# Kernel optimization log

Hardware: AMD Instinct MI355X
Metric: run time of the kernel (lower is better)

## Reference

```python
import jax, jax.numpy as jnp
import numpy as np

N, D, HID, IN_DIM, ED = 8192, 16, 128, 128, 8


def _lin(k, fi, fo):
    return jax.random.normal(k, (fi, fo), jnp.float32) / np.sqrt(fi).astype(np.float32)


def setup_inputs() -> dict:
    key = jax.random.key(0)
    ks = jax.random.split(key, 8)
    rng = np.random.default_rng(0)
    # DAG with topological order 0..N-1: node v in [1,N) gets D predecessors in [0, v)
    v_arr = np.arange(1, N)
    src = np.floor(rng.random((N - 1, D)) * v_arr[:, None]).astype(np.int64)  # [N-1, D]
    dst = np.repeat(v_arr, D)
    edge_index = jnp.asarray(np.stack([src.reshape(-1), dst]))  # [2, E]
    E = (N - 1) * D
    return {
        "x": jax.random.normal(ks[0], (N, IN_DIM), jnp.float32),
        "edge_index": edge_index,
        "edge_attr": jax.random.normal(ks[1], (E, ED), jnp.float32),
        "Wp": _lin(ks[2], IN_DIM, HID), "bp": jnp.zeros(HID, jnp.float32),
        "Wm1": _lin(ks[3], HID + ED, HID), "bm1": jnp.zeros(HID, jnp.float32),
        "Wm2": _lin(ks[4], HID, HID), "bm2": jnp.zeros(HID, jnp.float32),
        "Wu1": _lin(ks[5], 2 * HID, HID), "bu1": jnp.zeros(HID, jnp.float32),
        "Wu2": _lin(ks[6], HID, HID), "bu2": jnp.zeros(HID, jnp.float32),
    }


def _build_struct(edge_index, num_nodes):
    # Group edges by destination, padded to max in-degree (host-side, int constants)
    si, di = np.asarray(edge_index)
    order = np.argsort(di, kind="stable")
    si_s, di_s = si[order], di[order]
    deg = np.bincount(di_s, minlength=num_nodes)
    Dm = max(int(deg.max()), 1)
    offs = np.concatenate([[0], np.cumsum(deg)])
    pos = np.arange(di_s.shape[0]) - offs[di_s]  # slot of each edge within its dst group
    src_pad = np.zeros((num_nodes, Dm), np.int64)
    mask = np.zeros((num_nodes, Dm), np.float32)
    src_pad[di_s, pos] = si_s
    mask[di_s, pos] = 1.0
    return (jnp.asarray(src_pad), jnp.asarray(mask),
            jnp.asarray(order), jnp.asarray(di_s), jnp.asarray(pos), Dm)


def _forward(x, edge_attr, params, struct):
    Wp, bp, Wm1, bm1, Wm2, bm2, Wu1, bu1, Wu2, bu2 = params
    src_pad, mask, order, di_s, pos, Dm = struct
    num_nodes = x.shape[0]
    relu = jax.nn.relu
    # Scatter edge attrs into padded [N, Dm, ED] slots (differentiable w.r.t. edge_attr)
    attr_pad = jnp.zeros((num_nodes, Dm, edge_attr.shape[-1]), edge_attr.dtype)
    attr_pad = attr_pad.at[di_s, pos].set(edge_attr[order])
    h0 = x @ Wp + bp  # node_proj

    def step(h, inp):
        srcs, attr, m, v = inp
        hs = h[srcs]                                    # [Dm, HID] current (possibly updated) states
        z = jnp.concatenate([hs, attr], axis=-1)        # [Dm, HID+ED]
        msgs = relu(relu(z @ Wm1 + bm1) @ Wm2 + bm2)    # msg_mlp
        cnt = m.sum()
        agg = (msgs * m[:, None]).sum(0) / jnp.maximum(cnt, 1.0)  # masked mean
        cat = jnp.concatenate([h[v], agg])              # [2*HID]
        new = relu(relu(cat @ Wu1 + bu1) @ Wu2 + bu2)   # update_mlp
        h = h.at[v].set(jnp.where(cnt > 0, new, h[v]))  # skip nodes with no in-edges
        return h, None

    h, _ = jax.lax.scan(step, h0, (src_pad, attr_pad, mask, jnp.arange(num_nodes)))
    return h


def reference(x, edge_index, edge_attr, Wp, bp, Wm1, bm1, Wm2, bm2, Wu1, bu1, Wu2, bu2):
    struct = _build_struct(edge_index, x.shape[0])
    params = (Wp, bp, Wm1, bm1, Wm2, bm2, Wu1, bu1, Wu2, bu2)
    return _forward(x, edge_attr, params, struct)
```

## Files before the change

kernel.cpp:

```cpp
#include <hip/hip_runtime.h>

#define NN   8192
#define DEG  16
#define HID  128
#define IND  128
#define ED   8
#define NBLK 256

typedef __bf16 bf16_t;
typedef __bf16 bf16x8 __attribute__((ext_vector_type(8)));
typedef float  f32x4  __attribute__((ext_vector_type(4)));
typedef unsigned long long u64;

static __device__ __forceinline__ f32x4 mfma16(bf16x8 a, bf16x8 b, f32x4 c) {
  return __builtin_amdgcn_mfma_f32_16x16x32_bf16(a, b, c, 0, 0, 0);
}
static __device__ __forceinline__ unsigned short bfbits(bf16_t x) {
  return __builtin_bit_cast(unsigned short, x);
}
static __device__ __forceinline__ bf16_t bits2bf(unsigned short x) {
  return __builtin_bit_cast(bf16_t, x);
}
static __device__ __forceinline__ void bar_lds() {
  __builtin_amdgcn_sched_barrier(0);
  asm volatile("s_waitcnt lgkmcnt(0)" ::: "memory");
  __builtin_amdgcn_s_barrier();
  __builtin_amdgcn_sched_barrier(0);
}
static __device__ __forceinline__ void bar_full() {
  __builtin_amdgcn_sched_barrier(0);
  asm volatile("s_waitcnt vmcnt(0) lgkmcnt(0)" ::: "memory");
  __builtin_amdgcn_s_barrier();
  __builtin_amdgcn_sched_barrier(0);
}

__global__ __launch_bounds__(128) void k_h0(const float* __restrict__ x,
                                            const float* __restrict__ Wp,
                                            const float* __restrict__ bp,
                                            float* __restrict__ h,
                                            unsigned* __restrict__ h2u,
                                            int* __restrict__ flags, int fs,
                                            int sent) {
  __shared__ float sx[8][IND];
  const int t  = threadIdx.x;
  const int vb = blockIdx.x * 8;
  #pragma unroll
  for (int rr = 0; rr < 8; ++rr) sx[rr][t] = x[(size_t)(vb + rr) * IND + t];
  __syncthreads();
  float acc[8];
  const float bias = bp[t];
  #pragma unroll
  for (int rr = 0; rr < 8; ++rr) acc[rr] = bias;
  for (int k = 0; k < IND; ++k) {
    const float w = Wp[k * HID + t];
    #pragma unroll
    for (int rr = 0; rr < 8; ++rr) acc[rr] += sx[rr][k] * w;
  }
  #pragma unroll
  for (int rr = 0; rr < 8; ++rr) h[(size_t)(vb + rr) * HID + t] = acc[rr];
  if (sent) {
    #pragma unroll
    for (int rr = 0; rr < 8; ++rr) {
      unsigned val = 0xFFFFFFFFu;
      if (vb + rr == 0) {
        const float f = acc[rr];
        const bf16_t fh = (bf16_t)f;
        const bf16_t fl = (bf16_t)(f - (float)fh);
        val = ((unsigned)bfbits(fh) << 16) | (unsigned)bfbits(fl);
      }
      h2u[(size_t)(vb + rr) * HID + t] = val;
    }
  } else if (t < 8) {
    flags[(vb + t) * fs] = (vb + t == 0) ? 0xF : 0;
  }
}

#define LOAD_WFRAGS(W, KROWS, NKK, ARRH, ARRL)                                \
  _Pragma("unroll")                                                           \
  for (int n = 0; n < 2; ++n) {                                               \
    _Pragma("unroll")                                                         \
    for (int kk = 0; kk < NKK; ++kk) {                                        \
      _Pragma("unroll")                                                       \
      for (int i = 0; i < 8; ++i) {                                           \
        const int k = kk * 32 + g * 8 + i;                                    \
        const float w = (k < KROWS) ? W[k * HID + cc[n]] : 0.f;               \
        const bf16_t wh = (bf16_t)w;                                          \
        ARRH[n][kk][i] = wh;                                                  \
        ARRL[n][kk][i] = (bf16_t)(w - (float)wh);                             \
      }                                                                       \
    }                                                                         \
  }
#define LOAD_WFRAGS_H(W, KROWS, NKK, ARRH)                                    \
  _Pragma("unroll")                                                           \
  for (int n = 0; n < 2; ++n) {                                               \
    _Pragma("unroll")                                                         \
    for (int kk = 0; kk < NKK; ++kk) {                                        \
      _Pragma("unroll")                                                       \
      for (int i = 0; i < 8; ++i) {                                           \
        const int k = kk * 32 + g * 8 + i;                                    \
        const float w = (k < KROWS) ? W[k * HID + cc[n]] : 0.f;               \
        ARRH[n][kk][i] = (bf16_t)w;                                           \
      }                                                                       \
    }                                                                         \
  }

#define LOADQ()                                                               \
  _Pragma("unroll")                                                           \
  for (int kk = 0; kk < 4; ++kk) {                                            \
    _Pragma("unroll")                                                         \
    for (int u = 0; u < 4; ++u)                                               \
      q[kk * 4 + u] = __hip_atomic_load(hp + kk * 16 + u, __ATOMIC_RELAXED,   \
                                        __HIP_MEMORY_SCOPE_AGENT);            \
  }

#define ZERO4(a) { a[0][0]=0.f;a[0][1]=0.f;a[0][2]=0.f;a[0][3]=0.f; a[1]=a[0]; }
#define BIAS4(a, b) { a[0][0]=b[0];a[0][1]=b[0];a[0][2]=b[0];a[0][3]=b[0];    \
                      a[1][0]=b[1];a[1][1]=b[1];a[1][2]=b[1];a[1][3]=b[1]; }

template <bool SENT>
__global__ __launch_bounds__(256, 1) void k_dag(
    const int* __restrict__ ei, const float* __restrict__ attr,
    const float* __restrict__ Wm1, const float* __restrict__ bm1,
    const float* __restrict__ Wm2, const float* __restrict__ bm2,
    const float* __restrict__ Wu1, const float* __restrict__ bu1,
    const float* __restrict__ Wu2, const float* __restrict__ bu2,
    float* __restrict__ h, unsigned* __restrict__ h2u,
    int* __restrict__ flags, int fs) {
  const int tid  = threadIdx.x;
  const int lane = tid & 63;
  const int g    = lane >> 4;
  const int r    = lane & 15;
  const int wid  = tid >> 6;

  __shared__ bf16_t s_m1[16 * HID];
  __shared__ alignas(16) bf16_t s_agg[HID];
  __shared__ alignas(16) bf16_t s_u1[HID];

  int cc[2];
  cc[0] = wid * 32 + 2 * r;
  cc[1] = cc[0] + 1;

  bf16x8 wm1h[2][5], wm1l[2][5];
  bf16x8 wm2h[2][4];
  bf16x8 wu1h[2][8], wu1l[2][4];
  bf16x8 wu2h[2][4], wu2l[2][4];
  LOAD_WFRAGS(Wm1, 136, 5, wm1h, wm1l)
  LOAD_WFRAGS_H(Wm2, 128, 4, wm2h)
  LOAD_WFRAGS_H(Wu1, 256, 8, wu1h)
  LOAD_WFRAGS(Wu1, 128, 4, wu1h , wu1l)
  LOAD_WFRAGS(Wu2, 128, 4, wu2h, wu2l)
  float bs_m1[2], bs_m2[2], bs_u1[2], bs_u2[2];
  #pragma unroll
  for (int n = 0; n < 2; ++n) {
    bs_m1[n] = bm1[cc[n]]; bs_m2[n] = bm2[cc[n]];
    bs_u1[n] = bu1[cc[n]]; bs_u2[n] = bu2[cc[n]];
  }

  const int v0 = 1 + (int)blockIdx.x;
  int s_cur = (v0 < NN) ? ei[(v0 - 1) * DEG + r] : 0;

  for (int v = v0; v < NN; v += NBLK) {
    u64 q[16];
    const u64* hp =
        (const u64*)((SENT ? (const void*)h2u : (const void*)h)) +
        (size_t)s_cur * (HID / 2) + g * 4;
    LOADQ();

    const int vn = (v + NBLK < NN) ? v + NBLK : v;
    const int s_nxt = ei[(vn - 1) * DEG + r];

    bf16x8 hvh[4], hvl[4];
    {
      const float* hvp = h + (size_t)v * HID + g * 8;
      #pragma unroll
      for (int kk = 0; kk < 4; ++kk) {
        const f32x4 p0 = *(const f32x4*)(hvp + kk * 32);
        const f32x4 p1 = *(const f32x4*)(hvp + kk * 32 + 4);
        #pragma unroll
        for (int i = 0; i < 4; ++i) {
          const float f0 = p0[i], f1 = p1[i];
          const bf16_t f0h = (bf16_t)f0, f1h = (bf16_t)f1;
          hvh[kk][i]     = f0h; hvl[kk][i]     = (bf16_t)(f0 - (float)f0h);
          hvh[kk][4 + i] = f1h; hvl[kk][4 + i] = (bf16_t)(f1 - (float)f1h);
        }
      }
    }
    bf16x8 a4h;
    #pragma unroll
    for (int i = 0; i < 8; ++i) a4h[i] = (bf16_t)0.f;
    if (g == 0) {
      const f32x4* ap = (const f32x4*)(attr + ((size_t)(v - 1) * DEG + r) * ED);
      const f32x4 a0 = ap[0], a1 = ap[1];
      #pragma unroll
      for (int i = 0; i < 4; ++i) {
        a4h[i] = (bf16_t)a0[i]; a4h[4 + i] = (bf16_t)a1[i];
      }
    }

    f32x4 uA[2], uB[2], uC[2], uD[2];
    BIAS4(uA, bs_u1) ZERO4(uB) ZERO4(uC) ZERO4(uD)
    #pragma unroll
    for (int kk = 0; kk < 4; ++kk) {
      #pragma unroll
      for (int n = 0; n < 2; ++n) {
        uA[n] = mfma16(hvh[kk], wu1h[n][kk], uA[n]);
        uB[n] = mfma16(hvh[kk], wu1l[n][kk], uB[n]);
        uC[n] = mfma16(hvl[kk], wu1h[n][kk], uC[n]);
      }
    }
    f32x4 mA[2], mB[2], mC[2], mD[2], mE[2], mF[2];
    BIAS4(mA, bs_m1) ZERO4(mB) ZERO4(mC) ZERO4(mD) ZERO4(mE) ZERO4(mF)
    #pragma unroll
    for (int n = 0; n < 2; ++n) {
      mA[n] = mfma16(a4h, wm1h[n][4], mA[n]);
      mB[n] = mfma16(a4h, wm1l[n][4], mB[n]);
    }

    if constexpr (SENT) {
      bool ok = false;
      int guard = 0;
      for (;;) {
        if (!ok) {
          u64 m = 0;
          #pragma unroll
          for (int i = 0; i < 16; ++i) m |= q[i];
          ok = (s_cur == 0) || ((m & 0x8000000080000000ull) == 0);
        }
        if (__all(ok)) break;
        if (++guard > (1 << 13)) break;
        if (!ok) LOADQ();
      }
    } else {
      const int* fp = flags + s_cur * fs;
      int fw = __hip_atomic_load(fp, __ATOMIC_RELAXED, __HIP_MEMORY_SCOPE_AGENT);
      int guard = 0;
      while (fw != 0xF && ++guard < (1 << 15)) {
        __builtin_amdgcn_s_sleep(1);
        fw = __hip_atomic_load(fp, __ATOMIC_RELAXED, __HIP_MEMORY_SCOPE_AGENT);
      }
      asm volatile("" ::: "memory");
      LOADQ();
    }

    bf16x8 ah[4], al[4];
    #pragma unroll
    for (int kk = 0; kk < 4; ++kk) {
      #pragma unroll
      for (int u = 0; u < 4; ++u) {
        #pragma unroll
        for (int b = 0; b < 2; ++b) {
          const unsigned w = (unsigned)(q[kk * 4 + u] >> (32 * b));
          if constexpr (SENT) {
            ah[kk][u * 2 + b] = bits2bf((unsigned short)(w >> 16));
            al[kk][u * 2 + b] = bits2bf((unsigned short)(w & 0xFFFFu));
          } else {
            const float f = __uint_as_float(w);
            const bf16_t fh = (bf16_t)f;
            ah[kk][u * 2 + b] = fh;
            al[kk][u * 2 + b] = (bf16_t)(f - (float)fh);
          }
        }
      }
    }

    f32x4 m1[2];
    #pragma unroll
    for (int kk = 0; kk < 2; ++kk) {
      #pragma unroll
      for (int n = 0; n < 2; ++n) {
        mA[n] = mfma16(ah[kk], wm1h[n][kk], mA[n]);
        mB[n] = mfma16(ah[kk], wm1l[n][kk], mB[n]);
        mC[n] = mfma16(al[kk], wm1h[n][kk], mC[n]);
        mD[n] = mfma16(ah[kk + 2], wm1h[n][kk + 2], mD[n]);
        mE[n] = mfma16(ah[kk + 2], wm1l[n][kk + 2], mE[n]);
        mF[n] = mfma16(al[kk + 2], wm1h[n][kk + 2], mF[n]);
      }
    }
    #pragma unroll
    for (int n = 0; n < 2; ++n)
      m1[n] = ((mA[n] + mB[n]) + (mC[n] + mD[n])) + (mE[n] + mF[n]);
    #pragma unroll
    for (int n = 0; n < 2; ++n) {
      const int c = cc[n], ch16 = c >> 3;
      #pragma unroll
      for (int reg = 0; reg < 4; ++reg) {
        const int j = g * 4 + reg;
        s_m1[j * HID + ((ch16 ^ j) * 8) + (c & 7)] = (bf16_t)fmaxf(m1[n][reg], 0.f);
      }
    }
    if constexpr (SENT) bar_lds(); else __syncthreads();

    f32x4 m2[2];
    {
      f32x4 aA[2], aC[2];
      BIAS4(aA, bs_m2) ZERO4(aC)
      #pragma unroll
      for (int kk = 0; kk < 2; ++kk) {
        const int ph0 = (kk * 4 + g) ^ r;
        const int ph1 = ((kk + 2) * 4 + g) ^ r;
        const bf16x8 a0 = *(const bf16x8*)(s_m1 + r * HID + ph0 * 8);
        const bf16x8 a1 = *(const bf16x8*)(s_m1 + r * HID + ph1 * 8);
        #pragma unroll
        for (int n = 0; n < 2; ++n) {
          aA[n] = mfma16(a0, wm2h[n][kk], aA[n]);
          aC[n] = mfma16(a1, wm2h[n][kk + 2], aC[n]);
        }
      }
      #pragma unroll
      for (int n = 0; n < 2; ++n) m2[n] = aA[n] + aC[n];
    }
    #pragma unroll
    for (int n = 0; n < 2; ++n) {
      float s = fmaxf(m2[n][0],0.f)+fmaxf(m2[n][1],0.f)+fmaxf(m2[n][2],0.f)+fmaxf(m2[n][3],0.f);
      s += __shfl_xor(s, 16, 64);
      s += __shfl_xor(s, 32, 64);
      if (lane < 16) s_agg[cc[n]] = (bf16_t)(s * 0.0625f);
    }
    if constexpr (SENT) bar_lds(); else __syncthreads();

    f32x4 u1v[2];
    #pragma unroll
    for (int kk = 4; kk < 6; ++kk) {
      const bf16x8 Ah0 = *(const bf16x8*)(s_agg + (kk - 4) * 32 + g * 8);
      const bf16x8 Ah1 = *(const bf16x8*)(s_agg + (kk - 2) * 32 + g * 8);
      #pragma unroll
      for (int n = 0; n < 2; ++n) {
        uA[n] = mfma16(Ah0, wu1h[n][kk], uA[n]);
        uD[n] = mfma16(Ah1, wu1h[n][kk + 2], uD[n]);
      }
    }
    #pragma unroll
    for (int n = 0; n < 2; ++n)
      u1v[n] = (uA[n] + uB[n]) + (uC[n] + uD[n]);
    if (lane < 16) {
      s_u1[cc[0]] = (bf16_t)fmaxf(u1v[0][0], 0.f);
      s_u1[cc[1]] = (bf16_t)fmaxf(u1v[1][0], 0.f);
    }
    if constexpr (SENT) bar_lds(); else __syncthreads();

    f32x4 u2v[2];
    {
      f32x4 aA[2], aB[2], aC[2], aD[2];
      BIAS4(aA, bs_u2) ZERO4(aB) ZERO4(aC) ZERO4(aD)
      #pragma unroll
      for (int kk = 0; kk < 2; ++kk) {
        const bf16x8 Ah0 = *(const bf16x8*)(s_u1 + kk * 32 + g * 8);
        const bf16x8 Ah1 = *(const bf16x8*)(s_u1 + (kk + 2) * 32 + g * 8);
        #pragma unroll
        for (int n = 0; n < 2; ++n) {
          aA[n] = mfma16(Ah0, wu2h[n][kk], aA[n]);
          aB[n] = mfma16(Ah0, wu2l[n][kk], aB[n]);
          aC[n] = mfma16(Ah1, wu2h[n][kk + 2], aC[n]);
          aD[n] = mfma16(Ah1, wu2l[n][kk + 2], aD[n]);
        }
      }
      #pragma unroll
      for (int n = 0; n < 2; ++n) u2v[n] = (aA[n] + aB[n]) + (aC[n] + aD[n]);
    }
    if (lane < 16) {
      if constexpr (SENT) {
        u64 pp = 0;
        #pragma unroll
        for (int n = 0; n < 2; ++n) {
          const float rv = fabsf(fmaxf(u2v[n][0], 0.f));
          const bf16_t rh = (bf16_t)rv;
          const bf16_t rl = (bf16_t)(rv - (float)rh);
          const unsigned pw = ((unsigned)bfbits(rh) << 16) | (unsigned)bfbits(rl);
          pp |= (u64)pw << (32 * n);
        }
        __hip_atomic_store((u64*)&h2u[(size_t)v * HID + cc[0]], pp,
                           __ATOMIC_RELAXED, __HIP_MEMORY_SCOPE_AGENT);
      } else {
        #pragma unroll
        for (int n = 0; n < 2; ++n) {
          const float rv = fabsf(fmaxf(u2v[n][0], 0.f));
          __hip_atomic_store(&h[(size_t)v * HID + cc[n]], rv,
                             __ATOMIC_RELAXED, __HIP_MEMORY_SCOPE_AGENT);
        }
      }
    }
    if constexpr (!SENT) {
      if (lane == 0)
        __hip_atomic_fetch_or(&flags[v * fs], 1 << wid, __ATOMIC_RELEASE,
                              __HIP_MEMORY_SCOPE_AGENT);
    }
    s_cur = s_nxt;
    if constexpr (!SENT) __syncthreads();
  }

  if constexpr (SENT) {
    bar_full();
    const int half = tid >> 7;
    const int c    = tid & 127;
    #pragma unroll 4
    for (int v = v0 + half * NBLK; v < NN; v += 2 * NBLK) {
      const unsigned w = __hip_atomic_load(&h2u[(size_t)v * HID + c],
                                           __ATOMIC_RELAXED,
                                           __HIP_MEMORY_SCOPE_AGENT);
      h[(size_t)v * HID + c] =
          (float)bits2bf((unsigned short)(w >> 16)) +
          (float)bits2bf((unsigned short)(w & 0xFFFFu));
    }
  }
}

extern "C" void kernel_launch(void* const* d_in, const int* in_sizes, int n_in,
                              void* d_out, int out_size, void* d_ws, size_t ws_size,
                              hipStream_t stream) {
  const float* x    = (const float*)d_in[0];
  const int*   ei   = (const int*)  d_in[1];
  const float* attr = (const float*)d_in[2];
  const float* Wp   = (const float*)d_in[3];
  const float* bp   = (const float*)d_in[4];
  const float* Wm1  = (const float*)d_in[5];
  const float* bm1  = (const float*)d_in[6];
  const float* Wm2  = (const float*)d_in[7];
  const float* bm2  = (const float*)d_in[8];
  const float* Wu1  = (const float*)d_in[9];
  const float* bu1  = (const float*)d_in[10];
  const float* Wu2  = (const float*)d_in[11];
  const float* bu2  = (const float*)d_in[12];
  float* h = (float*)d_out;

  const size_t h2_bytes = (size_t)NN * HID * sizeof(unsigned);
  const bool sent = ws_size >= h2_bytes;
  unsigned* h2u = (unsigned*)d_ws;
  int* flags    = (int*)d_ws;
  const int fs = sent ? 0 : ((ws_size >= (size_t)NN * 64 + 64) ? 16 : 1);

  k_h0<<<NN / 8, 128, 0, stream>>>(x, Wp, bp, h, h2u, flags, fs, sent ? 1 : 0);
  if (sent)
    k_dag<true><<<NBLK, 256, 0, stream>>>(ei, attr, Wm1, bm1, Wm2, bm2,
                                          Wu1, bu1, Wu2, bu2, h, h2u, flags, fs);
  else
    k_dag<false><<<NBLK, 256, 0, stream>>>(ei, attr, Wm1, bm1, Wm2, bm2,
                                           Wu1, bu1, Wu2, bu2, h, h2u, flags, fs);
}
```

Before: 556.1 us.

## Split hi/lo bf16 planes and drop low-part gather in message matmul

```diff
diff --git a/kernel.cpp b/kernel.cpp
--- a/kernel.cpp
+++ b/kernel.cpp
@@ -11,6 +11,7 @@
 typedef __bf16 bf16x8 __attribute__((ext_vector_type(8)));
 typedef float  f32x4  __attribute__((ext_vector_type(4)));
 typedef unsigned long long u64;
+typedef u64 u64x2 __attribute__((ext_vector_type(2)));
 
 static __device__ __forceinline__ f32x4 mfma16(bf16x8 a, bf16x8 b, f32x4 c) {
   return __builtin_amdgcn_mfma_f32_16x16x32_bf16(a, b, c, 0, 0, 0);
@@ -38,7 +39,8 @@
                                             const float* __restrict__ Wp,
                                             const float* __restrict__ bp,
                                             float* __restrict__ h,
-                                            unsigned* __restrict__ h2u,
+                                            bf16_t* __restrict__ h2hi,
+                                            bf16_t* __restrict__ h2lo,
                                             int* __restrict__ flags, int fs,
                                             int sent) {
   __shared__ float sx[8][IND];
@@ -61,14 +63,15 @@
   if (sent) {
     #pragma unroll
     for (int rr = 0; rr < 8; ++rr) {
-      unsigned val = 0xFFFFFFFFu;
+      unsigned short hw = 0xFFFFu, lw = 0xFFFFu;
       if (vb + rr == 0) {
         const float f = acc[rr];
         const bf16_t fh = (bf16_t)f;
-        const bf16_t fl = (bf16_t)(f - (float)fh);
-        val = ((unsigned)bfbits(fh) << 16) | (unsigned)bfbits(fl);
-      }
-      h2u[(size_t)(vb + rr) * HID + t] = val;
+        hw = bfbits(fh);
+        lw = bfbits((bf16_t)(f - (float)fh));
+      }
+      h2hi[(size_t)(vb + rr) * HID + t] = bits2bf(hw);
+      h2lo[(size_t)(vb + rr) * HID + t] = bits2bf(lw);
     }
   } else if (t < 8) {
     flags[(vb + t) * fs] = (vb + t == 0) ? 0xF : 0;
@@ -103,13 +106,26 @@
       }                                                                       \
     }                                                                         \
   }
-
-#define LOADQ()                                                               \
+#define LOAD_WFRAGS_L(W, KROWS, NKK, ARRL)                                    \
+  _Pragma("unroll")                                                           \
+  for (int n = 0; n < 2; ++n) {                                               \
+    _Pragma("unroll")                                                         \
+    for (int kk = 0; kk < NKK; ++kk) {                                        \
+      _Pragma("unroll")                                                       \
+      for (int i = 0; i < 8; ++i) {                                           \
+        const int k = kk * 32 + g * 8 + i;                                    \
+        const float w = (k < KROWS) ? W[k * HID + cc[n]] : 0.f;               \
+        ARRL[n][kk][i] = (bf16_t)(w - (float)(bf16_t)w);                      \
+      }                                                                       \
+    }                                                                         \
+  }
+
+#define LOADQH()                                                              \
   _Pragma("unroll")                                                           \
   for (int kk = 0; kk < 4; ++kk) {                                            \
     _Pragma("unroll")                                                         \
-    for (int u = 0; u < 4; ++u)                                               \
-      q[kk * 4 + u] = __hip_atomic_load(hp + kk * 16 + u, __ATOMIC_RELAXED,   \
+    for (int u = 0; u < 2; ++u)                                               \
+      q[kk * 2 + u] = __hip_atomic_load(hp + kk * 8 + u, __ATOMIC_RELAXED,    \
                                         __HIP_MEMORY_SCOPE_AGENT);            \
   }
 
@@ -124,8 +140,8 @@
     const float* __restrict__ Wm2, const float* __restrict__ bm2,
     const float* __restrict__ Wu1, const float* __restrict__ bu1,
     const float* __restrict__ Wu2, const float* __restrict__ bu2,
-    float* __restrict__ h, unsigned* __restrict__ h2u,
-    int* __restrict__ flags, int fs) {
+    float* __restrict__ h, bf16_t* __restrict__ h2hi,
+    bf16_t* __restrict__ h2lo, int* __restrict__ flags, int fs) {
   const int tid  = threadIdx.x;
   const int lane = tid & 63;
   const int g    = lane >> 4;
@@ -147,7 +163,7 @@
   LOAD_WFRAGS(Wm1, 136, 5, wm1h, wm1l)
   LOAD_WFRAGS_H(Wm2, 128, 4, wm2h)
   LOAD_WFRAGS_H(Wu1, 256, 8, wu1h)
-  LOAD_WFRAGS(Wu1, 128, 4, wu1h , wu1l)
+  LOAD_WFRAGS_L(Wu1, 128, 4, wu1l)
   LOAD_WFRAGS(Wu2, 128, 4, wu2h, wu2l)
   float bs_m1[2], bs_m2[2], bs_u1[2], bs_u2[2];
   #pragma unroll
@@ -161,10 +177,19 @@
 
   for (int v = v0; v < NN; v += NBLK) {
     u64 q[16];
-    const u64* hp =
-        (const u64*)((SENT ? (const void*)h2u : (const void*)h)) +
-        (size_t)s_cur * (HID / 2) + g * 4;
-    LOADQ();
+    const u64* hp;
+    if constexpr (SENT) {
+      hp = (const u64*)(h2hi + (size_t)s_cur * HID) + g * 2;
+      LOADQH();
+    } else {
+      hp = (const u64*)(h + (size_t)s_cur * HID) + g * 4;
+      #pragma unroll
+      for (int kk = 0; kk < 4; ++kk)
+        #pragma unroll
+        for (int u = 0; u < 4; ++u)
+          q[kk * 4 + u] = __hip_atomic_load(hp + kk * 16 + u, __ATOMIC_RELAXED,
+                                            __HIP_MEMORY_SCOPE_AGENT);
+    }
 
     const int vn = (v + NBLK < NN) ? v + NBLK : v;
     const int s_nxt = ei[(vn - 1) * DEG + r];
@@ -208,8 +233,8 @@
         uC[n] = mfma16(hvl[kk], wu1h[n][kk], uC[n]);
       }
     }
-    f32x4 mA[2], mB[2], mC[2], mD[2], mE[2], mF[2];
-    BIAS4(mA, bs_m1) ZERO4(mB) ZERO4(mC) ZERO4(mD) ZERO4(mE) ZERO4(mF)
+    f32x4 mA[2], mB[2], mD[2], mE[2];
+    BIAS4(mA, bs_m1) ZERO4(mB) ZERO4(mD) ZERO4(mE)
     #pragma unroll
     for (int n = 0; n < 2; ++n) {
       mA[n] = mfma16(a4h, wm1h[n][4], mA[n]);
@@ -223,12 +248,12 @@
         if (!ok) {
           u64 m = 0;
           #pragma unroll
-          for (int i = 0; i < 16; ++i) m |= q[i];
-          ok = (s_cur == 0) || ((m & 0x8000000080000000ull) == 0);
+          for (int i = 0; i < 8; ++i) m |= q[i];
+          ok = (s_cur == 0) || ((m & 0x8000800080008000ull) == 0);
         }
         if (__all(ok)) break;
         if (++guard > (1 << 13)) break;
-        if (!ok) LOADQ();
+        if (!ok) LOADQH();
       }
     } else {
       const int* fp = flags + s_cur * fs;
@@ -239,27 +264,27 @@
         fw = __hip_atomic_load(fp, __ATOMIC_RELAXED, __HIP_MEMORY_SCOPE_AGENT);
       }
       asm volatile("" ::: "memory");
-      LOADQ();
-    }
-
-    bf16x8 ah[4], al[4];
+      #pragma unroll
+      for (int kk = 0; kk < 4; ++kk)
+        #pragma unroll
+        for (int u = 0; u < 4; ++u)
+          q[kk * 4 + u] = __hip_atomic_load(hp + kk * 16 + u, __ATOMIC_RELAXED,
+                                            __HIP_MEMORY_SCOPE_AGENT);
+    }
+
+    bf16x8 ah[4];
     #pragma unroll
     for (int kk = 0; kk < 4; ++kk) {
-      #pragma unroll
-      for (int u = 0; u < 4; ++u) {
-        #pragma unroll
-        for (int b = 0; b < 2; ++b) {
-          const unsigned w = (unsigned)(q[kk * 4 + u] >> (32 * b));
-          if constexpr (SENT) {
-            ah[kk][u * 2 + b] = bits2bf((unsigned short)(w >> 16));
-            al[kk][u * 2 + b] = bits2bf((unsigned short)(w & 0xFFFFu));
-          } else {
-            const float f = __uint_as_float(w);
-            const bf16_t fh = (bf16_t)f;
-            ah[kk][u * 2 + b] = fh;
-            al[kk][u * 2 + b] = (bf16_t)(f - (float)fh);
-          }
-        }
+      if constexpr (SENT) {
+        u64x2 t2; t2[0] = q[kk * 2]; t2[1] = q[kk * 2 + 1];
+        ah[kk] = __builtin_bit_cast(bf16x8, t2);
+      } else {
+        #pragma unroll
+        for (int u = 0; u < 4; ++u)
+          #pragma unroll
+          for (int b = 0; b < 2; ++b)
+            ah[kk][u * 2 + b] =
+                (bf16_t)__uint_as_float((unsigned)(q[kk * 4 + u] >> (32 * b)));
       }
     }
 
@@ -270,15 +295,12 @@
       for (int n = 0; n < 2; ++n) {
         mA[n] = mfma16(ah[kk], wm1h[n][kk], mA[n]);
         mB[n] = mfma16(ah[kk], wm1l[n][kk], mB[n]);
-        mC[n] = mfma16(al[kk], wm1h[n][kk], mC[n]);
         mD[n] = mfma16(ah[kk + 2], wm1h[n][kk + 2], mD[n]);
         mE[n] = mfma16(ah[kk + 2], wm1l[n][kk + 2], mE[n]);
-        mF[n] = mfma16(al[kk + 2], wm1h[n][kk + 2], mF[n]);
-      }
-    }
-    #pragma unroll
-    for (int n = 0; n < 2; ++n)
-      m1[n] = ((mA[n] + mB[n]) + (mC[n] + mD[n])) + (mE[n] + mF[n]);
+      }
+    }
+    #pragma unroll
+    for (int n = 0; n < 2; ++n) m1[n] = (mA[n] + mB[n]) + (mD[n] + mE[n]);
     #pragma unroll
     for (int n = 0; n < 2; ++n) {
       const int c = cc[n], ch16 = c >> 3;
@@ -359,16 +381,16 @@
     }
     if (lane < 16) {
       if constexpr (SENT) {
-        u64 pp = 0;
-        #pragma unroll
-        for (int n = 0; n < 2; ++n) {
-          const float rv = fabsf(fmaxf(u2v[n][0], 0.f));
-          const bf16_t rh = (bf16_t)rv;
-          const bf16_t rl = (bf16_t)(rv - (float)rh);
-          const unsigned pw = ((unsigned)bfbits(rh) << 16) | (unsigned)bfbits(rl);
-          pp |= (u64)pw << (32 * n);
-        }
-        __hip_atomic_store((u64*)&h2u[(size_t)v * HID + cc[0]], pp,
+        const float r0 = fabsf(fmaxf(u2v[0][0], 0.f));
+        const float r1 = fabsf(fmaxf(u2v[1][0], 0.f));
+        const bf16_t h0b = (bf16_t)r0, h1b = (bf16_t)r1;
+        const unsigned hiw = (unsigned)bfbits(h0b) | ((unsigned)bfbits(h1b) << 16);
+        const unsigned low = (unsigned)bfbits((bf16_t)(r0 - (float)h0b)) |
+                             ((unsigned)bfbits((bf16_t)(r1 - (float)h1b)) << 16);
+        const size_t wi = (size_t)v * (HID / 2) + wid * 16 + r;
+        __hip_atomic_store((unsigned*)h2lo + wi, low,
+                           __ATOMIC_RELAXED, __HIP_MEMORY_SCOPE_AGENT);
+        __hip_atomic_store((unsigned*)h2hi + wi, hiw,
                            __ATOMIC_RELAXED, __HIP_MEMORY_SCOPE_AGENT);
       } else {
         #pragma unroll
@@ -390,16 +412,23 @@
 
   if constexpr (SENT) {
     bar_full();
-    const int half = tid >> 7;
-    const int c    = tid & 127;
-    #pragma unroll 4
-    for (int v = v0 + half * NBLK; v < NN; v += 2 * NBLK) {
-      const unsigned w = __hip_atomic_load(&h2u[(size_t)v * HID + c],
-                                           __ATOMIC_RELAXED,
-                                           __HIP_MEMORY_SCOPE_AGENT);
-      h[(size_t)v * HID + c] =
-          (float)bits2bf((unsigned short)(w >> 16)) +
-          (float)bits2bf((unsigned short)(w & 0xFFFFu));
+    const unsigned* hi32 = (const unsigned*)h2hi;
+    const unsigned* lo32 = (const unsigned*)h2lo;
+    const int sub = tid >> 6;
+    const int c2  = tid & 63;
+    for (int v = v0 + sub * NBLK; v < NN; v += 4 * NBLK) {
+      const unsigned hw = __hip_atomic_load(&hi32[(size_t)v * 64 + c2],
+                                            __ATOMIC_RELAXED,
+                                            __HIP_MEMORY_SCOPE_AGENT);
+      const unsigned lw = __hip_atomic_load(&lo32[(size_t)v * 64 + c2],
+                                            __ATOMIC_RELAXED,
+                                            __HIP_MEMORY_SCOPE_AGENT);
+      h[(size_t)v * HID + 2 * c2] =
+          (float)bits2bf((unsigned short)(hw & 0xFFFF)) +
+          (float)bits2bf((unsigned short)(lw & 0xFFFF));
+      h[(size_t)v * HID + 2 * c2 + 1] =
+          (float)bits2bf((unsigned short)(hw >> 16)) +
+          (float)bits2bf((unsigned short)(lw >> 16));
     }
   }
 }
@@ -422,17 +451,21 @@
   const float* bu2  = (const float*)d_in[12];
   float* h = (float*)d_out;
 
-  const size_t h2_bytes = (size_t)NN * HID * sizeof(unsigned);
-  const bool sent = ws_size >= h2_bytes;
-  unsigned* h2u = (unsigned*)d_ws;
-  int* flags    = (int*)d_ws;
+  const size_t plane = (size_t)NN * HID * sizeof(bf16_t);
+  const bool sent = ws_size >= 2 * plane;
+  bf16_t* h2hi = (bf16_t*)d_ws;
+  bf16_t* h2lo = (bf16_t*)((char*)d_ws + plane);
+  int* flags   = (int*)d_ws;
   const int fs = sent ? 0 : ((ws_size >= (size_t)NN * 64 + 64) ? 16 : 1);
 
-  k_h0<<<NN / 8, 128, 0, stream>>>(x, Wp, bp, h, h2u, flags, fs, sent ? 1 : 0);
+  k_h0<<<NN / 8, 128, 0, stream>>>(x, Wp, bp, h, h2hi, h2lo, flags, fs,
+                                   sent ? 1 : 0);
   if (sent)
     k_dag<true><<<NBLK, 256, 0, stream>>>(ei, attr, Wm1, bm1, Wm2, bm2,
-                                          Wu1, bu1, Wu2, bu2, h, h2u, flags, fs);
+                                          Wu1, bu1, Wu2, bu2, h, h2hi, h2lo,
+                                          flags, fs);
   else
     k_dag<false><<<NBLK, 256, 0, stream>>>(ei, attr, Wm1, bm1, Wm2, bm2,
-                                           Wu1, bu1, Wu2, bu2, h, h2u, flags, fs);
-}
+                                           Wu1, bu1, Wu2, bu2, h, h2hi, h2lo,
+                                           flags, fs);
+}
```

New measurement: 508.5 us. -8.6%, faster.
